# Kernel optimization log

Measured on AMD Instinct MI355X. Metric: run time of the kernel, lower is better.

Reference implementation:

```python
import jax, jax.numpy as jnp
import numpy as np

D = 1      # d (problem dimension); code is only consistent for d=1
H = 5      # hidden_size (hard-coded in TwoLayerLSTMOptimizer)
M = 3      # polynomial degree m
GAMMA = 0.99
B = 1_048_576


def setup_inputs() -> dict:
    key = jax.random.key(0)
    ks = jax.random.split(key, 20)
    def n(k, shape, s=1.0):
        return jax.random.normal(k, shape, dtype=jnp.float32) * s
    return {
        "bx": n(ks[0], (B, D)),
        "bl": n(ks[1], (B, D)),
        "bg": n(ks[2], (B, D)),
        # LSTMCell 1: input_size = 2*D+1 = 3
        "W_ih1": n(ks[3], (4 * H, 2 * D + 1), 0.3),
        "W_hh1": n(ks[4], (4 * H, H), 0.3),
        "b_ih1": n(ks[5], (4 * H,), 0.1),
        "b_hh1": n(ks[6], (4 * H,), 0.1),
        # LSTMCell 2: input_size = H
        "W_ih2": n(ks[7], (4 * H, H), 0.3),
        "W_hh2": n(ks[8], (4 * H, H), 0.3),
        "b_ih2": n(ks[9], (4 * H,), 0.1),
        "b_hh2": n(ks[10], (4 * H,), 0.1),
        # output layer: H -> D
        "W_out": n(ks[11], (D, H), 0.3),
        "b_out": n(ks[12], (D,), 0.1),
        # learned initial states (batch dim 1, broadcast over B)
        "h1_0": n(ks[13], (1, H), 0.01),
        "c1_0": n(ks[14], (1, H), 0.01),
        "h2_0": n(ks[15], (1, H), 0.01),
        "c2_0": n(ks[16], (1, H), 0.01),
        "poly_coefficients": jnp.full((M + 1,), -2.0, dtype=jnp.float32),
        "t": 0,
    }


def _lstm_cell(u, h, c, W_ih, W_hh, b_ih, b_hh):
    # torch.nn.LSTMCell gate math, vectorized over the batch
    gates = u @ W_ih.T + b_ih + h @ W_hh.T + b_hh  # [B, 4H]
    i, f, g, o = jnp.split(gates, 4, axis=-1)
    c_new = jax.nn.sigmoid(f) * c + jax.nn.sigmoid(i) * jnp.tanh(g)
    h_new = jax.nn.sigmoid(o) * jnp.tanh(c_new)
    return h_new, c_new


def _inf_norm_scale(v):
    # v / ||v||_inf when norm > 0, else v
    nrm = jnp.max(jnp.abs(v), axis=-1, keepdims=True)  # [B, 1]
    safe = jnp.where(nrm > 0, nrm, 1.0)
    return jnp.where(nrm > 0, v / safe, v), nrm


def reference(bx, bl, bg, W_ih1, W_hh1, b_ih1, b_hh1,
              W_ih2, W_hh2, b_ih2, b_hh2, W_out, b_out,
              h1_0, c1_0, h2_0, c2_0, poly_coefficients, t):
    xn, nx = _inf_norm_scale(bx)
    ln, _ = _inf_norm_scale(bl)
    gn, _ = _inf_norm_scale(bg)
    # per-sample u is [D, 3] with D=1 -> stack features: [B, 2D+1]
    u = jnp.concatenate([xn, ln, gn], axis=-1)  # [B, 3]

    h1, c1 = _lstm_cell(u, h1_0, c1_0, W_ih1, W_hh1, b_ih1, b_hh1)
    h2, c2 = _lstm_cell(h1, h2_0, c2_0, W_ih2, W_hh2, b_ih2, b_hh2)
    v = h2 @ W_out.T + b_out          # [B, D]
    v = jnp.tanh(v) * jnp.where(nx > 0, nx, 1.0)  # rescale by ||bx||_inf if > 0

    # poly_value = softplus(coeffs) . [t^0, ..., t^m];  t is a static Python int
    t_powers = jnp.asarray([float(t) ** j for j in range(M + 1)], dtype=jnp.float32)
    poly_value = jnp.dot(jax.nn.softplus(poly_coefficients), t_powers)
    bv = poly_value * v * (GAMMA ** t)
    return bv
```

## Files before the change

### kernel.cpp

```cpp
#include <hip/hip_runtime.h>
#include <math.h>

#define HID 5
#define NTAB 27

__device__ __forceinline__ float sigm(float x) { return 1.0f / (1.0f + expf(-x)); }
__device__ __forceinline__ float softplus_f(float x) {
    return fmaxf(x, 0.0f) + log1pf(expf(-fabsf(x)));
}

__device__ __forceinline__ float sample_out(const float* __restrict__ tab,
                                            float x, float l, float g) {
    int sx = (x > 0.0f) - (x < 0.0f);
    int sl = (l > 0.0f) - (l < 0.0f);
    int sg = (g > 0.0f) - (g < 0.0f);
    float ax = fabsf(x);
    float scale = (ax > 0.0f) ? ax : 1.0f;
    return tab[(sx + 1) * 9 + (sl + 1) * 3 + (sg + 1)] * scale;
}

__global__ __launch_bounds__(256) void lstm_opt_kernel(
    const float* __restrict__ bx, const float* __restrict__ bl, const float* __restrict__ bg,
    const float* __restrict__ W_ih1, const float* __restrict__ W_hh1,
    const float* __restrict__ b_ih1, const float* __restrict__ b_hh1,
    const float* __restrict__ W_ih2, const float* __restrict__ W_hh2,
    const float* __restrict__ b_ih2, const float* __restrict__ b_hh2,
    const float* __restrict__ W_out, const float* __restrict__ b_out,
    const float* __restrict__ h1_0, const float* __restrict__ c1_0,
    const float* __restrict__ h2_0, const float* __restrict__ c2_0,
    const float* __restrict__ poly, const int* __restrict__ t_ptr,
    float* __restrict__ out, int N)
{
    __shared__ float s_table[NTAB];
    const int tid = threadIdx.x;

    if (tid < NTAB) {
        float gn = (float)(tid % 3) - 1.0f;
        float ln = (float)((tid / 3) % 3) - 1.0f;
        float xn = (float)(tid / 9) - 1.0f;

        float h1[HID];
        for (int j = 0; j < HID; ++j) {
            float gk[4];
            #pragma unroll
            for (int q = 0; q < 4; ++q) {
                int k = j + q * HID;
                float acc = b_ih1[k] + b_hh1[k];
                #pragma unroll
                for (int m = 0; m < HID; ++m) acc += W_hh1[k * HID + m] * h1_0[m];
                acc += W_ih1[k * 3 + 0] * xn + W_ih1[k * 3 + 1] * ln + W_ih1[k * 3 + 2] * gn;
                gk[q] = acc;
            }
            float c = sigm(gk[1]) * c1_0[j] + sigm(gk[0]) * tanhf(gk[2]);
            h1[j] = sigm(gk[3]) * tanhf(c);
        }

        float h2v[HID];
        for (int j = 0; j < HID; ++j) {
            float gk[4];
            #pragma unroll
            for (int q = 0; q < 4; ++q) {
                int k = j + q * HID;
                float acc = b_ih2[k] + b_hh2[k];
                #pragma unroll
                for (int m = 0; m < HID; ++m) acc += W_hh2[k * HID + m] * h2_0[m];
                #pragma unroll
                for (int m = 0; m < HID; ++m) acc += W_ih2[k * HID + m] * h1[m];
                gk[q] = acc;
            }
            float c = sigm(gk[1]) * c2_0[j] + sigm(gk[0]) * tanhf(gk[2]);
            h2v[j] = sigm(gk[3]) * tanhf(c);
        }

        float v = b_out[0];
        #pragma unroll
        for (int m = 0; m < HID; ++m) v += W_out[m] * h2v[m];

        int t = *t_ptr;
        float tf = (float)t;
        float pv = 0.0f, p = 1.0f;
        #pragma unroll
        for (int jj = 0; jj < 4; ++jj) { pv += softplus_f(poly[jj]) * p; p *= tf; }
        float gt = powf(0.99f, tf);

        s_table[tid] = pv * gt * tanhf(v);
    }
    __syncthreads();

    const int gtid = blockIdx.x * blockDim.x + tid;
    const int gstride = gridDim.x * blockDim.x;
    const int nvec = N >> 2;

    const float4* bx4 = reinterpret_cast<const float4*>(bx);
    const float4* bl4 = reinterpret_cast<const float4*>(bl);
    const float4* bg4 = reinterpret_cast<const float4*>(bg);
    float4* out4 = reinterpret_cast<float4*>(out);

    for (int i = gtid; i < nvec; i += gstride) {
        float4 x = bx4[i];
        float4 l = bl4[i];
        float4 g = bg4[i];
        float4 o;
        o.x = sample_out(s_table, x.x, l.x, g.x);
        o.y = sample_out(s_table, x.y, l.y, g.y);
        o.z = sample_out(s_table, x.z, l.z, g.z);
        o.w = sample_out(s_table, x.w, l.w, g.w);
        out4[i] = o;
    }
    for (int i = (nvec << 2) + gtid; i < N; i += gstride) {
        out[i] = sample_out(s_table, bx[i], bl[i], bg[i]);
    }
}

extern "C" void kernel_launch(void* const* d_in, const int* in_sizes, int n_in,
                              void* d_out, int out_size, void* d_ws, size_t ws_size,
                              hipStream_t stream) {
    const float* bx    = (const float*)d_in[0];
    const float* bl    = (const float*)d_in[1];
    const float* bg    = (const float*)d_in[2];
    const float* W_ih1 = (const float*)d_in[3];
    const float* W_hh1 = (const float*)d_in[4];
    const float* b_ih1 = (const float*)d_in[5];
    const float* b_hh1 = (const float*)d_in[6];
    const float* W_ih2 = (const float*)d_in[7];
    const float* W_hh2 = (const float*)d_in[8];
    const float* b_ih2 = (const float*)d_in[9];
    const float* b_hh2 = (const float*)d_in[10];
    const float* W_out = (const float*)d_in[11];
    const float* b_out = (const float*)d_in[12];
    const float* h1_0  = (const float*)d_in[13];
    const float* c1_0  = (const float*)d_in[14];
    const float* h2_0  = (const float*)d_in[15];
    const float* c2_0  = (const float*)d_in[16];
    const float* poly  = (const float*)d_in[17];
    const int*   t_ptr = (const int*)d_in[18];
    float* out = (float*)d_out;

    int N = in_sizes[0];
    int nvec = N >> 2;
    int blocks = (nvec + 255) / 256;
    if (blocks < 1) blocks = 1;
    if (blocks > 2048) blocks = 2048;

    lstm_opt_kernel<<<blocks, 256, 0, stream>>>(
        bx, bl, bg, W_ih1, W_hh1, b_ih1, b_hh1,
        W_ih2, W_hh2, b_ih2, b_hh2, W_out, b_out,
        h1_0, c1_0, h2_0, c2_0, poly, t_ptr, out, N);
}
```

Measured before the change: 15.91 us.

## Compute lookup table per wavefront and overlap first input loads with table build

Each wavefront now builds the 27-entry output table redundantly in its lanes and reads entries with a wave shuffle, replacing the shared-memory table and block barrier. The first float4 loads are issued before the LSTM table computation so global memory latency overlaps the arithmetic. powf is swapped for exp2f with a precomputed log2 constant. The cost is that every lane, not just 27 threads, runs the full LSTM math, which adds ALU work per wave.

```diff
diff --git a/kernel.cpp b/kernel.cpp
--- a/kernel.cpp
+++ b/kernel.cpp
@@ -9,17 +9,17 @@
     return fmaxf(x, 0.0f) + log1pf(expf(-fabsf(x)));
 }
 
-__device__ __forceinline__ float sample_out(const float* __restrict__ tab,
-                                            float x, float l, float g) {
+__device__ __forceinline__ float samp(float tval, float x, float l, float g) {
     int sx = (x > 0.0f) - (x < 0.0f);
     int sl = (l > 0.0f) - (l < 0.0f);
     int sg = (g > 0.0f) - (g < 0.0f);
+    int idx = (sx + 1) * 9 + (sl + 1) * 3 + (sg + 1);
+    float tv = __shfl(tval, idx, 64);
     float ax = fabsf(x);
-    float scale = (ax > 0.0f) ? ax : 1.0f;
-    return tab[(sx + 1) * 9 + (sl + 1) * 3 + (sg + 1)] * scale;
+    return tv * ((ax > 0.0f) ? ax : 1.0f);
 }
 
-__global__ __launch_bounds__(256) void lstm_opt_kernel(
+__global__ __launch_bounds__(256) void lstm_opt_wave(
     const float* __restrict__ bx, const float* __restrict__ bl, const float* __restrict__ bg,
     const float* __restrict__ W_ih1, const float* __restrict__ W_hh1,
     const float* __restrict__ b_ih1, const float* __restrict__ b_hh1,
@@ -31,15 +31,30 @@
     const float* __restrict__ poly, const int* __restrict__ t_ptr,
     float* __restrict__ out, int N)
 {
-    __shared__ float s_table[NTAB];
     const int tid = threadIdx.x;
+    const int lane = tid & 63;
 
-    if (tid < NTAB) {
-        float gn = (float)(tid % 3) - 1.0f;
-        float ln = (float)((tid / 3) % 3) - 1.0f;
-        float xn = (float)(tid / 9) - 1.0f;
+    const int gtid = blockIdx.x * blockDim.x + tid;
+    const int gstride = gridDim.x * blockDim.x;
+    const int nvec = N >> 2;
+
+    const float4* bx4 = reinterpret_cast<const float4*>(bx);
+    const float4* bl4 = reinterpret_cast<const float4*>(bl);
+    const float4* bg4 = reinterpret_cast<const float4*>(bg);
+    float4* out4 = reinterpret_cast<float4*>(out);
+
+    float4 x0, l0, g0;
+    bool have0 = (gtid < nvec);
+    if (have0) { x0 = bx4[gtid]; l0 = bl4[gtid]; g0 = bg4[gtid]; }
+
+    {
+        int li = (lane < NTAB) ? lane : 0;
+        float gn = (float)(li % 3) - 1.0f;
+        float ln = (float)((li / 3) % 3) - 1.0f;
+        float xn = (float)(li / 9) - 1.0f;
 
         float h1[HID];
+        #pragma unroll
         for (int j = 0; j < HID; ++j) {
             float gk[4];
             #pragma unroll
@@ -56,6 +71,7 @@
         }
 
         float h2v[HID];
+        #pragma unroll
         for (int j = 0; j < HID; ++j) {
             float gk[4];
             #pragma unroll
@@ -81,34 +97,32 @@
         float pv = 0.0f, p = 1.0f;
         #pragma unroll
         for (int jj = 0; jj < 4; ++jj) { pv += softplus_f(poly[jj]) * p; p *= tf; }
-        float gt = powf(0.99f, tf);
+        float gt = exp2f(tf * -0.0144995696951150f);
 
-        s_table[tid] = pv * gt * tanhf(v);
-    }
-    __syncthreads();
+        float tval = pv * gt * tanhf(v);
 
-    const int gtid = blockIdx.x * blockDim.x + tid;
-    const int gstride = gridDim.x * blockDim.x;
-    const int nvec = N >> 2;
-
-    const float4* bx4 = reinterpret_cast<const float4*>(bx);
-    const float4* bl4 = reinterpret_cast<const float4*>(bl);
-    const float4* bg4 = reinterpret_cast<const float4*>(bg);
-    float4* out4 = reinterpret_cast<float4*>(out);
-
-    for (int i = gtid; i < nvec; i += gstride) {
-        float4 x = bx4[i];
-        float4 l = bl4[i];
-        float4 g = bg4[i];
-        float4 o;
-        o.x = sample_out(s_table, x.x, l.x, g.x);
-        o.y = sample_out(s_table, x.y, l.y, g.y);
-        o.z = sample_out(s_table, x.z, l.z, g.z);
-        o.w = sample_out(s_table, x.w, l.w, g.w);
-        out4[i] = o;
-    }
-    for (int i = (nvec << 2) + gtid; i < N; i += gstride) {
-        out[i] = sample_out(s_table, bx[i], bl[i], bg[i]);
+        if (have0) {
+            float4 o;
+            o.x = samp(tval, x0.x, l0.x, g0.x);
+            o.y = samp(tval, x0.y, l0.y, g0.y);
+            o.z = samp(tval, x0.z, l0.z, g0.z);
+            o.w = samp(tval, x0.w, l0.w, g0.w);
+            out4[gtid] = o;
+        }
+        for (int i = gtid + gstride; i < nvec; i += gstride) {
+            float4 x = bx4[i];
+            float4 l = bl4[i];
+            float4 g = bg4[i];
+            float4 o;
+            o.x = samp(tval, x.x, l.x, g.x);
+            o.y = samp(tval, x.y, l.y, g.y);
+            o.z = samp(tval, x.z, l.z, g.z);
+            o.w = samp(tval, x.w, l.w, g.w);
+            out4[i] = o;
+        }
+        for (int i = (nvec << 2) + gtid; i < N; i += gstride) {
+            out[i] = samp(tval, bx[i], bl[i], bg[i]);
+        }
     }
 }
 
@@ -142,7 +156,7 @@
     if (blocks < 1) blocks = 1;
     if (blocks > 2048) blocks = 2048;
 
-    lstm_opt_kernel<<<blocks, 256, 0, stream>>>(
+    lstm_opt_wave<<<blocks, 256, 0, stream>>>(
         bx, bl, bg, W_ih1, W_hh1, b_ih1, b_hh1,
         W_ih2, W_hh2, b_ih2, b_hh2, W_out, b_out,
         h1_0, c1_0, h2_0, c2_0, poly, t_ptr, out, N);
```

Measured after the change: 23.60 us. +48.4%, slower.
